# Kernel optimization log

Measured on AMD Instinct MI355X. Metric: run time of the kernel, lower is better.

The kernel has to match this reference:

```python
import jax, jax.numpy as jnp
import numpy as np

B, N, K, D = 256, 100, 16, 128


def setup_inputs() -> dict:
    key = jax.random.key(0)
    k1, k2, k3, k4, k5, k6, k7 = jax.random.split(key, 7)
    return {
        "self_vectors": jax.random.normal(k1, (B, N, D), jnp.float32),
        "neighbor_vector": jax.random.normal(k2, (B, N, K, D), jnp.float32),
        "neighbor_weight": jax.random.uniform(k3, (B, N, K), jnp.float32),
        "extra_vector": jax.random.normal(k4, (B, N, D), jnp.float32),
        "w_1": jax.random.normal(k5, (D + 1, D), jnp.float32) / np.sqrt(D + 1),
        "w_2": jax.random.normal(k6, (D, 1), jnp.float32) / np.sqrt(D),
        "w_3": jax.random.normal(k7, (2 * D, D), jnp.float32) / np.sqrt(2 * D),
        "batch_size": B,
    }


def reference(self_vectors, neighbor_vector, neighbor_weight, extra_vector, w_1, w_2, w_3, batch_size):
    # attention branch (extra_vector is not None)
    feat = extra_vector[:, :, None, :] * neighbor_vector           # [B,N,K,D]
    feat = jnp.concatenate([feat, neighbor_weight[..., None]], -1)  # [B,N,K,D+1]
    alpha = jnp.einsum('bnkf,fd->bnkd', feat, w_1)                  # [B,N,K,D]
    alpha = jax.nn.leaky_relu(alpha, negative_slope=0.2)
    alpha = jnp.einsum('bnkd,do->bnk', alpha, w_2)                  # [B,N,K]
    alpha = jax.nn.softmax(alpha, axis=-1)[..., None]               # [B,N,K,1]
    agg = jnp.sum(alpha * neighbor_vector, axis=-2)                 # [B,N,D]
    # combine (dropout is identity in eval mode / p=0)
    out = jnp.concatenate([self_vectors, agg], axis=-1) @ w_3       # [B,N,D]
    out = out.reshape(batch_size, -1, w_3.shape[1])
    return jax.nn.relu(out)
```

## Files before the change

kernel.cpp:

```cpp
#include <hip/hip_runtime.h>
#include <stdint.h>

#define BN_TOTAL 25600
#define DDIM 128
#define KN 16

typedef __bf16 bf16x8 __attribute__((ext_vector_type(8)));
typedef float f32x4 __attribute__((ext_vector_type(4)));
typedef float f32x16 __attribute__((ext_vector_type(16)));
typedef unsigned short u16x8 __attribute__((ext_vector_type(8)));

__device__ __forceinline__ unsigned short f2bf(float x) {
    unsigned int u = __builtin_bit_cast(unsigned int, x);
    u = (u + 0x7fffu + ((u >> 16) & 1u)) >> 16;
    return (unsigned short)u;
}

__device__ __forceinline__ void gload_lds16(const void* g, void* l) {
    __builtin_amdgcn_global_load_lds(
        (const __attribute__((address_space(1))) void*)g,
        (__attribute__((address_space(3))) void*)l, 16, 0, 0);
}

__global__ __launch_bounds__(256) void k0_build_frags(
    const float* __restrict__ w1,
    const float* __restrict__ w3,
    uint4* __restrict__ fw1,
    uint4* __restrict__ fw3)
{
    const int slot = blockIdx.x * 256 + threadIdx.x;
    if (slot < 2048) {
        const int idx  = slot >> 6;
        const int lane = slot & 63;
        const int t = idx >> 2, s = idx & 3;
        const int grp = lane >> 4, lr = lane & 15;
        const int fbase = grp * 8 + 32 * s;
        const int d = t * 16 + lr;
        u16x8 tmp;
        #pragma unroll
        for (int j = 0; j < 8; ++j)
            tmp[j] = f2bf(w1[(fbase + j) * DDIM + d]);
        fw1[slot] = __builtin_bit_cast(uint4, tmp);
    } else {
        const int q = slot - 2048;
        const int idx  = q >> 6;
        const int lane = q & 63;
        const int t = idx >> 3, s = idx & 7;
        const int grp = lane >> 4, lr = lane & 15;
        const int fbase = grp * 8 + 32 * s;
        const int d = t * 16 + lr;
        u16x8 tmp;
        #pragma unroll
        for (int j = 0; j < 8; ++j)
            tmp[j] = f2bf(w3[(fbase + j) * DDIM + d]);
        fw3[q] = __builtin_bit_cast(uint4, tmp);
    }
}

__global__ __launch_bounds__(256) void k1_attn_agg(
    const float* __restrict__ nbr,
    const float* __restrict__ wgt,
    const float* __restrict__ extra,
    const float* __restrict__ w1,
    const float* __restrict__ w2,
    const uint4* __restrict__ fw1,
    unsigned short* __restrict__ aggb)
{
    __shared__ uint4 b1frag[32][64];
    __shared__ float w1last[DDIM];
    __shared__ float w2s[DDIM];

    const int tid  = threadIdx.x;
    const int lane = tid & 63;
    const int wave = tid >> 6;
    const int grp  = lane >> 4;
    const int lr   = lane & 15;
    const int half = lane >> 5;
    const int col  = lane & 31;

    #pragma unroll
    for (int c = 0; c < 8; ++c)
        gload_lds16(fw1 + (wave * 8 + c) * 64 + lane, &b1frag[wave * 8 + c][0]);
    if (tid < DDIM) {
        w1last[tid] = w1[DDIM * DDIM + tid];
        w2s[tid]    = w2[tid];
    }
    __syncthreads();

    const int bn = blockIdx.x * 4 + wave;
    const float* nb = nbr   + (size_t)bn * (KN * DDIM);
    const float* ex = extra + (size_t)bn * DDIM;

    const float4 wv = *(const float4*)(wgt + (size_t)bn * KN + grp * 4);
    f32x4 acc[8];
    #pragma unroll
    for (int t = 0; t < 8; ++t) {
        const float wl = w1last[t * 16 + lr];
        acc[t][0] = wv.x * wl;
        acc[t][1] = wv.y * wl;
        acc[t][2] = wv.z * wl;
        acc[t][3] = wv.w * wl;
    }

    #pragma unroll
    for (int s = 0; s < 4; ++s) {
        const int f0 = grp * 8 + 32 * s;
        const float4 n0 = *(const float4*)(nb + lr * DDIM + f0);
        const float4 n1 = *(const float4*)(nb + lr * DDIM + f0 + 4);
        const float4 e0 = *(const float4*)(ex + f0);
        const float4 e1 = *(const float4*)(ex + f0 + 4);
        u16x8 au;
        au[0] = f2bf(n0.x * e0.x); au[1] = f2bf(n0.y * e0.y);
        au[2] = f2bf(n0.z * e0.z); au[3] = f2bf(n0.w * e0.w);
        au[4] = f2bf(n1.x * e1.x); au[5] = f2bf(n1.y * e1.y);
        au[6] = f2bf(n1.z * e1.z); au[7] = f2bf(n1.w * e1.w);
        const bf16x8 af = __builtin_bit_cast(bf16x8, au);
        #pragma unroll
        for (int t = 0; t < 8; ++t) {
            const bf16x8 bf = __builtin_bit_cast(bf16x8, b1frag[t * 4 + s][lane]);
            acc[t] = __builtin_amdgcn_mfma_f32_16x16x32_bf16(af, bf, acc[t], 0, 0, 0);
        }
    }

    float b2raw[4][8];
    #pragma unroll
    for (int t = 0; t < 4; ++t)
        #pragma unroll
        for (int j = 0; j < 8; ++j)
            b2raw[t][j] = nb[(half * 8 + j) * DDIM + t * 32 + col];

    float sum0 = 0.f, sum1 = 0.f, sum2 = 0.f, sum3 = 0.f;
    #pragma unroll
    for (int t = 0; t < 8; ++t) {
        const float w2v = w2s[t * 16 + lr];
        float h;
        h = acc[t][0]; h = fmaxf(h, 0.2f * h); sum0 = fmaf(h, w2v, sum0);
        h = acc[t][1]; h = fmaxf(h, 0.2f * h); sum1 = fmaf(h, w2v, sum1);
        h = acc[t][2]; h = fmaxf(h, 0.2f * h); sum2 = fmaf(h, w2v, sum2);
        h = acc[t][3]; h = fmaxf(h, 0.2f * h); sum3 = fmaf(h, w2v, sum3);
    }
    #pragma unroll
    for (int m = 1; m <= 8; m <<= 1) {
        sum0 += __shfl_xor(sum0, m, 64);
        sum1 += __shfl_xor(sum1, m, 64);
        sum2 += __shfl_xor(sum2, m, 64);
        sum3 += __shfl_xor(sum3, m, 64);
    }
    float mx = fmaxf(fmaxf(sum0, sum1), fmaxf(sum2, sum3));
    mx = fmaxf(mx, __shfl_xor(mx, 16, 64));
    mx = fmaxf(mx, __shfl_xor(mx, 32, 64));
    const float ev0 = __expf(sum0 - mx);
    const float ev1 = __expf(sum1 - mx);
    const float ev2 = __expf(sum2 - mx);
    const float ev3 = __expf(sum3 - mx);
    float es = ev0 + ev1 + ev2 + ev3;
    es += __shfl_xor(es, 16, 64);
    es += __shfl_xor(es, 32, 64);
    const float inv = 1.0f / es;

    u16x8 a2u;
    #pragma unroll
    for (int j = 0; j < 8; ++j) {
        const int src = (((half * 8 + j) >> 2) << 4);
        float av;
        switch (j & 3) {
            case 0: av = __shfl(ev0, src, 64); break;
            case 1: av = __shfl(ev1, src, 64); break;
            case 2: av = __shfl(ev2, src, 64); break;
            default: av = __shfl(ev3, src, 64); break;
        }
        a2u[j] = f2bf(av * inv);
    }
    const bf16x8 a2 = __builtin_bit_cast(bf16x8, a2u);

    f32x16 z;
    #pragma unroll
    for (int i = 0; i < 16; ++i) z[i] = 0.f;

    unsigned short* ao = aggb + (size_t)bn * DDIM;
    #pragma unroll
    for (int t = 0; t < 4; ++t) {
        u16x8 bu;
        #pragma unroll
        for (int j = 0; j < 8; ++j) bu[j] = f2bf(b2raw[t][j]);
        const bf16x8 b2 = __builtin_bit_cast(bf16x8, bu);
        const f32x16 r = __builtin_amdgcn_mfma_f32_32x32x16_bf16(a2, b2, z, 0, 0, 0);
        if (lane < 32) ao[t * 32 + col] = f2bf(r[0]);
    }
}

__global__ __launch_bounds__(256) void k2_out_gemm(
    const float* __restrict__ selfv,
    const unsigned short* __restrict__ aggb,
    const uint4* __restrict__ fw3,
    float* __restrict__ out)
{
    __shared__ uint4 w3frag[64][64];

    const int tid  = threadIdx.x;
    const int lane = tid & 63;
    const int wave = tid >> 6;
    const int grp  = lane >> 4;
    const int lr   = lane & 15;

    #pragma unroll
    for (int c = 0; c < 16; ++c)
        gload_lds16(fw3 + (wave * 16 + c) * 64 + lane, &w3frag[wave * 16 + c][0]);
    __syncthreads();

    const int rowbase = blockIdx.x * 64 + wave * 16;
    const int row = rowbase + lr;

    f32x4 acc[8];
    #pragma unroll
    for (int t = 0; t < 8; ++t) {
        acc[t][0] = 0.f; acc[t][1] = 0.f; acc[t][2] = 0.f; acc[t][3] = 0.f;
    }

    #pragma unroll
    for (int s = 0; s < 8; ++s) {
        bf16x8 af;
        if (s < 4) {
            const int f0 = grp * 8 + 32 * s;
            const float4 x0 = *(const float4*)(selfv + (size_t)row * DDIM + f0);
            const float4 x1 = *(const float4*)(selfv + (size_t)row * DDIM + f0 + 4);
            u16x8 au;
            au[0] = f2bf(x0.x); au[1] = f2bf(x0.y); au[2] = f2bf(x0.z); au[3] = f2bf(x0.w);
            au[4] = f2bf(x1.x); au[5] = f2bf(x1.y); au[6] = f2bf(x1.z); au[7] = f2bf(x1.w);
            af = __builtin_bit_cast(bf16x8, au);
        } else {
            const int f0 = grp * 8 + 32 * (s - 4);
            const uint4 av = *(const uint4*)(aggb + (size_t)row * DDIM + f0);
            af = __builtin_bit_cast(bf16x8, av);
        }
        #pragma unroll
        for (int t = 0; t < 8; ++t) {
            const bf16x8 bf = __builtin_bit_cast(bf16x8, w3frag[t * 8 + s][lane]);
            acc[t] = __builtin_amdgcn_mfma_f32_16x16x32_bf16(af, bf, acc[t], 0, 0, 0);
        }
    }

    #pragma unroll
    for (int t = 0; t < 8; ++t) {
        #pragma unroll
        for (int j = 0; j < 4; ++j) {
            const int r = rowbase + grp * 4 + j;
            out[(size_t)r * DDIM + t * 16 + lr] = fmaxf(acc[t][j], 0.0f);
        }
    }
}

extern "C" void kernel_launch(void* const* d_in, const int* in_sizes, int n_in,
                              void* d_out, int out_size, void* d_ws, size_t ws_size,
                              hipStream_t stream)
{
    const float* selfv = (const float*)d_in[0];
    const float* nbr   = (const float*)d_in[1];
    const float* wgt   = (const float*)d_in[2];
    const float* extra = (const float*)d_in[3];
    const float* w1    = (const float*)d_in[4];
    const float* w2    = (const float*)d_in[5];
    const float* w3    = (const float*)d_in[6];
    float* out = (float*)d_out;

    unsigned short* aggb = (unsigned short*)d_ws;
    uint4* fw1 = (uint4*)((char*)d_ws + (8u << 20));
    uint4* fw3 = (uint4*)((char*)d_ws + (8u << 20) + (128u << 10));

    hipLaunchKernelGGL(k0_build_frags, dim3(24), dim3(256), 0, stream, w1, w3, fw1, fw3);
    hipLaunchKernelGGL(k1_attn_agg, dim3(6400), dim3(256), 0, stream,
                       nbr, wgt, extra, w1, w2, fw1, aggb);
    hipLaunchKernelGGL(k2_out_gemm, dim3(400), dim3(256), 0, stream,
                       selfv, aggb, fw3, out);
}
```

Baseline: 71.52 us.

## Use native bf16 conversion, prefetch first neighbor tile, drop LDS staging in out GEMM

Replaces the manual round-to-nearest bf16 conversion with native __bf16 casts, which may map to hardware convert instructions. In the attention kernel, the first slice of neighbor and extra data is now loaded before the LDS fill and barrier so those loads overlap the weight staging. The output GEMM now uses one-wave blocks that read W3 fragments straight from global memory and L2 instead of staging them in LDS, quadrupling the grid size. This removes the LDS fill and barrier but makes every wave re-read the whole W3 fragment set from cache.

```diff
diff --git a/kernel.cpp b/kernel.cpp
--- a/kernel.cpp
+++ b/kernel.cpp
@@ -8,13 +8,6 @@
 typedef __bf16 bf16x8 __attribute__((ext_vector_type(8)));
 typedef float f32x4 __attribute__((ext_vector_type(4)));
 typedef float f32x16 __attribute__((ext_vector_type(16)));
-typedef unsigned short u16x8 __attribute__((ext_vector_type(8)));
-
-__device__ __forceinline__ unsigned short f2bf(float x) {
-    unsigned int u = __builtin_bit_cast(unsigned int, x);
-    u = (u + 0x7fffu + ((u >> 16) & 1u)) >> 16;
-    return (unsigned short)u;
-}
 
 __device__ __forceinline__ void gload_lds16(const void* g, void* l) {
     __builtin_amdgcn_global_load_lds(
@@ -25,8 +18,8 @@
 __global__ __launch_bounds__(256) void k0_build_frags(
     const float* __restrict__ w1,
     const float* __restrict__ w3,
-    uint4* __restrict__ fw1,
-    uint4* __restrict__ fw3)
+    bf16x8* __restrict__ fw1,
+    bf16x8* __restrict__ fw3)
 {
     const int slot = blockIdx.x * 256 + threadIdx.x;
     if (slot < 2048) {
@@ -36,11 +29,11 @@
         const int grp = lane >> 4, lr = lane & 15;
         const int fbase = grp * 8 + 32 * s;
         const int d = t * 16 + lr;
-        u16x8 tmp;
+        bf16x8 tmp;
         #pragma unroll
         for (int j = 0; j < 8; ++j)
-            tmp[j] = f2bf(w1[(fbase + j) * DDIM + d]);
-        fw1[slot] = __builtin_bit_cast(uint4, tmp);
+            tmp[j] = (__bf16)w1[(fbase + j) * DDIM + d];
+        fw1[slot] = tmp;
     } else {
         const int q = slot - 2048;
         const int idx  = q >> 6;
@@ -49,11 +42,11 @@
         const int grp = lane >> 4, lr = lane & 15;
         const int fbase = grp * 8 + 32 * s;
         const int d = t * 16 + lr;
-        u16x8 tmp;
+        bf16x8 tmp;
         #pragma unroll
         for (int j = 0; j < 8; ++j)
-            tmp[j] = f2bf(w3[(fbase + j) * DDIM + d]);
-        fw3[q] = __builtin_bit_cast(uint4, tmp);
+            tmp[j] = (__bf16)w3[(fbase + j) * DDIM + d];
+        fw3[q] = tmp;
     }
 }
 
@@ -63,10 +56,10 @@
     const float* __restrict__ extra,
     const float* __restrict__ w1,
     const float* __restrict__ w2,
-    const uint4* __restrict__ fw1,
+    const bf16x8* __restrict__ fw1,
     unsigned short* __restrict__ aggb)
 {
-    __shared__ uint4 b1frag[32][64];
+    __shared__ bf16x8 b1frag[32][64];
     __shared__ float w1last[DDIM];
     __shared__ float w2s[DDIM];
 
@@ -78,6 +71,16 @@
     const int half = lane >> 5;
     const int col  = lane & 31;
 
+    const int bn = blockIdx.x * 4 + wave;
+    const float* nb = nbr   + (size_t)bn * (KN * DDIM);
+    const float* ex = extra + (size_t)bn * DDIM;
+
+    const float4 wv   = *(const float4*)(wgt + (size_t)bn * KN + grp * 4);
+    const float4 p_n0 = *(const float4*)(nb + lr * DDIM + grp * 8);
+    const float4 p_n1 = *(const float4*)(nb + lr * DDIM + grp * 8 + 4);
+    const float4 p_e0 = *(const float4*)(ex + grp * 8);
+    const float4 p_e1 = *(const float4*)(ex + grp * 8 + 4);
+
     #pragma unroll
     for (int c = 0; c < 8; ++c)
         gload_lds16(fw1 + (wave * 8 + c) * 64 + lane, &b1frag[wave * 8 + c][0]);
@@ -87,11 +90,6 @@
     }
     __syncthreads();
 
-    const int bn = blockIdx.x * 4 + wave;
-    const float* nb = nbr   + (size_t)bn * (KN * DDIM);
-    const float* ex = extra + (size_t)bn * DDIM;
-
-    const float4 wv = *(const float4*)(wgt + (size_t)bn * KN + grp * 4);
     f32x4 acc[8];
     #pragma unroll
     for (int t = 0; t < 8; ++t) {
@@ -105,29 +103,30 @@
     #pragma unroll
     for (int s = 0; s < 4; ++s) {
         const int f0 = grp * 8 + 32 * s;
-        const float4 n0 = *(const float4*)(nb + lr * DDIM + f0);
-        const float4 n1 = *(const float4*)(nb + lr * DDIM + f0 + 4);
-        const float4 e0 = *(const float4*)(ex + f0);
-        const float4 e1 = *(const float4*)(ex + f0 + 4);
-        u16x8 au;
-        au[0] = f2bf(n0.x * e0.x); au[1] = f2bf(n0.y * e0.y);
-        au[2] = f2bf(n0.z * e0.z); au[3] = f2bf(n0.w * e0.w);
-        au[4] = f2bf(n1.x * e1.x); au[5] = f2bf(n1.y * e1.y);
-        au[6] = f2bf(n1.z * e1.z); au[7] = f2bf(n1.w * e1.w);
-        const bf16x8 af = __builtin_bit_cast(bf16x8, au);
-        #pragma unroll
-        for (int t = 0; t < 8; ++t) {
-            const bf16x8 bf = __builtin_bit_cast(bf16x8, b1frag[t * 4 + s][lane]);
-            acc[t] = __builtin_amdgcn_mfma_f32_16x16x32_bf16(af, bf, acc[t], 0, 0, 0);
-        }
-    }
-
-    float b2raw[4][8];
+        float4 n0, n1, e0, e1;
+        if (s == 0) { n0 = p_n0; n1 = p_n1; e0 = p_e0; e1 = p_e1; }
+        else {
+            n0 = *(const float4*)(nb + lr * DDIM + f0);
+            n1 = *(const float4*)(nb + lr * DDIM + f0 + 4);
+            e0 = *(const float4*)(ex + f0);
+            e1 = *(const float4*)(ex + f0 + 4);
+        }
+        bf16x8 af;
+        af[0] = (__bf16)(n0.x * e0.x); af[1] = (__bf16)(n0.y * e0.y);
+        af[2] = (__bf16)(n0.z * e0.z); af[3] = (__bf16)(n0.w * e0.w);
+        af[4] = (__bf16)(n1.x * e1.x); af[5] = (__bf16)(n1.y * e1.y);
+        af[6] = (__bf16)(n1.z * e1.z); af[7] = (__bf16)(n1.w * e1.w);
+        #pragma unroll
+        for (int t = 0; t < 8; ++t)
+            acc[t] = __builtin_amdgcn_mfma_f32_16x16x32_bf16(af, b1frag[t * 4 + s][lane], acc[t], 0, 0, 0);
+    }
+
+    bf16x8 b2f[4];
     #pragma unroll
     for (int t = 0; t < 4; ++t)
         #pragma unroll
         for (int j = 0; j < 8; ++j)
-            b2raw[t][j] = nb[(half * 8 + j) * DDIM + t * 32 + col];
+            b2f[t][j] = (__bf16)nb[(half * 8 + j) * DDIM + t * 32 + col];
 
     float sum0 = 0.f, sum1 = 0.f, sum2 = 0.f, sum3 = 0.f;
     #pragma unroll
@@ -158,7 +157,7 @@
     es += __shfl_xor(es, 32, 64);
     const float inv = 1.0f / es;
 
-    u16x8 a2u;
+    bf16x8 a2;
     #pragma unroll
     for (int j = 0; j < 8; ++j) {
         const int src = (((half * 8 + j) >> 2) << 4);
@@ -169,9 +168,8 @@
             case 2: av = __shfl(ev2, src, 64); break;
             default: av = __shfl(ev3, src, 64); break;
         }
-        a2u[j] = f2bf(av * inv);
-    }
-    const bf16x8 a2 = __builtin_bit_cast(bf16x8, a2u);
+        a2[j] = (__bf16)(av * inv);
+    }
 
     f32x16 z;
     #pragma unroll
@@ -180,35 +178,24 @@
     unsigned short* ao = aggb + (size_t)bn * DDIM;
     #pragma unroll
     for (int t = 0; t < 4; ++t) {
-        u16x8 bu;
-        #pragma unroll
-        for (int j = 0; j < 8; ++j) bu[j] = f2bf(b2raw[t][j]);
-        const bf16x8 b2 = __builtin_bit_cast(bf16x8, bu);
-        const f32x16 r = __builtin_amdgcn_mfma_f32_32x32x16_bf16(a2, b2, z, 0, 0, 0);
-        if (lane < 32) ao[t * 32 + col] = f2bf(r[0]);
-    }
-}
-
-__global__ __launch_bounds__(256) void k2_out_gemm(
+        const f32x16 r = __builtin_amdgcn_mfma_f32_32x32x16_bf16(a2, b2f[t], z, 0, 0, 0);
+        if (lane < 32) {
+            const __bf16 rb = (__bf16)r[0];
+            ao[t * 32 + col] = __builtin_bit_cast(unsigned short, rb);
+        }
+    }
+}
+
+__global__ __launch_bounds__(64) void k2_out_gemm(
     const float* __restrict__ selfv,
     const unsigned short* __restrict__ aggb,
-    const uint4* __restrict__ fw3,
+    const bf16x8* __restrict__ fw3,
     float* __restrict__ out)
 {
-    __shared__ uint4 w3frag[64][64];
-
-    const int tid  = threadIdx.x;
-    const int lane = tid & 63;
-    const int wave = tid >> 6;
+    const int lane = threadIdx.x;
     const int grp  = lane >> 4;
     const int lr   = lane & 15;
-
-    #pragma unroll
-    for (int c = 0; c < 16; ++c)
-        gload_lds16(fw3 + (wave * 16 + c) * 64 + lane, &w3frag[wave * 16 + c][0]);
-    __syncthreads();
-
-    const int rowbase = blockIdx.x * 64 + wave * 16;
+    const int rowbase = blockIdx.x * 16;
     const int row = rowbase + lr;
 
     f32x4 acc[8];
@@ -217,6 +204,7 @@
         acc[t][0] = 0.f; acc[t][1] = 0.f; acc[t][2] = 0.f; acc[t][3] = 0.f;
     }
 
+    const bf16x8* fp = fw3 + lane;
     #pragma unroll
     for (int s = 0; s < 8; ++s) {
         bf16x8 af;
@@ -224,20 +212,17 @@
             const int f0 = grp * 8 + 32 * s;
             const float4 x0 = *(const float4*)(selfv + (size_t)row * DDIM + f0);
             const float4 x1 = *(const float4*)(selfv + (size_t)row * DDIM + f0 + 4);
-            u16x8 au;
-            au[0] = f2bf(x0.x); au[1] = f2bf(x0.y); au[2] = f2bf(x0.z); au[3] = f2bf(x0.w);
-            au[4] = f2bf(x1.x); au[5] = f2bf(x1.y); au[6] = f2bf(x1.z); au[7] = f2bf(x1.w);
-            af = __builtin_bit_cast(bf16x8, au);
+            af[0] = (__bf16)x0.x; af[1] = (__bf16)x0.y;
+            af[2] = (__bf16)x0.z; af[3] = (__bf16)x0.w;
+            af[4] = (__bf16)x1.x; af[5] = (__bf16)x1.y;
+            af[6] = (__bf16)x1.z; af[7] = (__bf16)x1.w;
         } else {
             const int f0 = grp * 8 + 32 * (s - 4);
-            const uint4 av = *(const uint4*)(aggb + (size_t)row * DDIM + f0);
-            af = __builtin_bit_cast(bf16x8, av);
-        }
-        #pragma unroll
-        for (int t = 0; t < 8; ++t) {
-            const bf16x8 bf = __builtin_bit_cast(bf16x8, w3frag[t * 8 + s][lane]);
-            acc[t] = __builtin_amdgcn_mfma_f32_16x16x32_bf16(af, bf, acc[t], 0, 0, 0);
-        }
+            af = *(const bf16x8*)(aggb + (size_t)row * DDIM + f0);
+        }
+        #pragma unroll
+        for (int t = 0; t < 8; ++t)
+            acc[t] = __builtin_amdgcn_mfma_f32_16x16x32_bf16(af, fp[(t * 8 + s) * 64], acc[t], 0, 0, 0);
     }
 
     #pragma unroll
@@ -264,12 +249,12 @@
     float* out = (float*)d_out;
 
     unsigned short* aggb = (unsigned short*)d_ws;
-    uint4* fw1 = (uint4*)((char*)d_ws + (8u << 20));
-    uint4* fw3 = (uint4*)((char*)d_ws + (8u << 20) + (128u << 10));
+    bf16x8* fw1 = (bf16x8*)((char*)d_ws + (8u << 20));
+    bf16x8* fw3 = (bf16x8*)((char*)d_ws + (8u << 20) + (128u << 10));
 
     hipLaunchKernelGGL(k0_build_frags, dim3(24), dim3(256), 0, stream, w1, w3, fw1, fw3);
     hipLaunchKernelGGL(k1_attn_agg, dim3(6400), dim3(256), 0, stream,
                        nbr, wgt, extra, w1, w2, fw1, aggb);
-    hipLaunchKernelGGL(k2_out_gemm, dim3(400), dim3(256), 0, stream,
+    hipLaunchKernelGGL(k2_out_gemm, dim3(1600), dim3(64), 0, stream,
                        selfv, aggb, fw3, out);
 }
```

New measurement: 75.29 us. 5.3% more time.
